# Kernel tuning notes

Measured on AMD Instinct MI355X. Metric: run time of the kernel, lower is better.

The kernel has to match this reference:

```python
import jax, jax.numpy as jnp
import numpy as np

B, H, W = 8, 64, 64
D_MODEL, D_STATE, D_INNER, DT_RANK, K = 96, 16, 192, 6, 4
EPS = 1e-6


def setup_inputs() -> dict:
    key = jax.random.key(0)
    ks = jax.random.split(key, 9)
    f = lambda k, s, sc=0.02: jax.random.normal(k, s, dtype=jnp.float32) * sc
    return {
        "x": jax.random.normal(ks[0], (B, H, W, D_MODEL), jnp.float32),
        "in_proj_w": f(ks[1], (2 * D_INNER, D_MODEL)),
        "conv_w": f(ks[2], (D_INNER, 1, 3, 3), 0.1),
        "conv_b": jnp.zeros((D_INNER,), jnp.float32),
        "x_proj_w": f(ks[3], (K * (DT_RANK + 2 * D_STATE), D_INNER)),
        "dt_projs_w": f(ks[4], (K * D_INNER, DT_RANK), 0.1),
        "A_logs": jnp.log(jax.random.uniform(ks[5], (K * D_INNER, D_STATE), jnp.float32, 1.0, 16.0)),
        "Ds": jnp.ones((K * D_INNER,), jnp.float32),
        "dt_projs_bias": f(ks[6], (K * D_INNER,), 0.5),
        "norm_w": jnp.ones((D_INNER,), jnp.float32),
        "norm_b": jnp.zeros((D_INNER,), jnp.float32),
        "out_proj_w": f(ks[7], (D_MODEL, D_INNER)),
    }


def _ss2d(x, in_proj_w, conv_w, conv_b, x_proj_w, dt_projs_w, A_logs, Ds,
          dt_projs_bias, norm_w, norm_b, out_proj_w):
    silu = jax.nn.silu
    Bb, Hh, Ww, _ = x.shape
    L = Hh * Ww
    # in_proj, split x/z, z gate activation
    xz = x @ in_proj_w.T                                   # (B,H,W,2*Di)
    xx, z = jnp.split(xz, 2, axis=-1)
    z = silu(z)
    # depthwise conv 3x3 in NCHW
    xc = jnp.transpose(xx, (0, 3, 1, 2))                   # (B,Di,H,W)
    xc = jax.lax.conv_general_dilated(
        xc, conv_w, (1, 1), ((1, 1), (1, 1)),
        dimension_numbers=("NCHW", "OIHW", "NCHW"),
        feature_group_count=D_INNER) + conv_b[None, :, None, None]
    xc = silu(xc)
    # 4-way cross scan: hw, wh (transposed), and their reversals
    x_hw = xc.reshape(Bb, D_INNER, L)
    x_wh = jnp.transpose(xc, (0, 1, 3, 2)).reshape(Bb, D_INNER, L)
    xs = jnp.stack([x_hw, x_wh, x_hw[..., ::-1], x_wh[..., ::-1]], axis=1)  # (B,K,Di,L)
    # per-group projections for dt, B, C
    xpw = x_proj_w.reshape(K, DT_RANK + 2 * D_STATE, D_INNER)
    x_dbl = jnp.einsum("bkdl,kcd->bkcl", xs, xpw)
    dts, Bs, Cs = jnp.split(x_dbl, [DT_RANK, DT_RANK + D_STATE], axis=2)
    dtw = dt_projs_w.reshape(K, D_INNER, DT_RANK)
    dts = jnp.einsum("bkrl,kdr->bkdl", dts, dtw)           # (B,K,Di,L)
    A = -jnp.exp(A_logs).reshape(K, D_INNER, D_STATE)      # (K,Di,N)
    dt = jax.nn.softplus(dts + dt_projs_bias.reshape(1, K, D_INNER, 1))
    # selective scan over L
    def step(h, inp):
        u_t, dt_t, B_t, C_t = inp                          # (B,K,Di),(B,K,Di),(B,K,N),(B,K,N)
        dA = jnp.exp(dt_t[..., None] * A)                  # (B,K,Di,N)
        h = h * dA + (dt_t * u_t)[..., None] * B_t[:, :, None, :]
        y = jnp.einsum("bkdn,bkn->bkd", h, C_t)
        return h, y
    h0 = jnp.zeros((Bb, K, D_INNER, D_STATE), jnp.float32)
    seq = (jnp.moveaxis(xs, -1, 0), jnp.moveaxis(dt, -1, 0),
           jnp.moveaxis(Bs, -1, 0), jnp.moveaxis(Cs, -1, 0))
    _, ysL = jax.lax.scan(step, h0, seq)
    ys = jnp.moveaxis(ysL, 0, -1)                          # (B,K,Di,L)
    ys = ys + xs * Ds.reshape(1, K, D_INNER, 1)
    # cross merge: invert flips and wh-transpose, then sum the 4 directions
    y = ys[:, 0] + ys[:, 2][..., ::-1]
    yw = ys[:, 1] + ys[:, 3][..., ::-1]
    y = y + yw.reshape(Bb, D_INNER, Ww, Hh).transpose(0, 1, 3, 2).reshape(Bb, D_INNER, L)
    y = y.reshape(Bb, D_INNER, Hh, Ww).transpose(0, 2, 3, 1)   # (B,H,W,Di)
    # out LayerNorm over channels
    mean = y.mean(-1, keepdims=True)
    var = ((y - mean) ** 2).mean(-1, keepdims=True)
    y = (y - mean) / jnp.sqrt(var + EPS) * norm_w + norm_b
    # gate and out_proj
    y = y * z
    return y @ out_proj_w.T                                # (B,H,W,d_model)


def reference(x, in_proj_w, conv_w, conv_b, x_proj_w, dt_projs_w, A_logs, Ds,
              dt_projs_bias, norm_w, norm_b, out_proj_w):
    return _ss2d(x, in_proj_w, conv_w, conv_b, x_proj_w, dt_projs_w, A_logs, Ds,
                 dt_projs_bias, norm_w, norm_b, out_proj_w)
```

## Files before the change

### kernel.cpp

```cpp
#include <hip/hip_runtime.h>
#include <hip/hip_bf16.h>
#include <math.h>

#define BB 8
#define HS 64
#define WS 64
#define LL 4096
#define DM 96
#define DI 192
#define NS 16
#define RR 6
#define KK 4
#define NCH 64
#define LC 64
#define XP 16
#define EPSN 1e-6f

typedef __attribute__((ext_vector_type(2))) float f32x2;

__device__ __forceinline__ float fsilu(float x) { return x / (1.f + __expf(-x)); }
__device__ __forceinline__ float rexp2(float x) {
    float r; asm("v_exp_f32 %0, %1" : "=v"(r) : "v"(x)); return r;
}
__device__ __forceinline__ float rlog2(float x) {
    float r; asm("v_log_f32 %0, %1" : "=v"(r) : "v"(x)); return r;
}
__device__ __forceinline__ f32x2 pk_mul(f32x2 a, f32x2 b) {
    f32x2 d; asm("v_pk_mul_f32 %0, %1, %2" : "=v"(d) : "v"(a), "v"(b)); return d;
}
__device__ __forceinline__ f32x2 pk_fma(f32x2 a, f32x2 b, f32x2 c) {
    f32x2 d; asm("v_pk_fma_f32 %0, %1, %2, %3" : "=v"(d) : "v"(a), "v"(b), "v"(c)); return d;
}
__device__ __forceinline__ float fsoftplus(float x) {
    float t = rexp2(x * 1.44269504f);
    float r = 0.69314718f * rlog2(1.f + t);
    return (x > 20.f) ? x : r;
}
__device__ __forceinline__ int lmap(int k, int t) {
    int tt = (k >= 2) ? (LL - 1 - t) : t;
    if (k & 1) tt = ((tt & 63) << 6) | (tt >> 6);
    return tt;
}

__global__ __launch_bounds__(192) void k_inproj(const float* __restrict__ x,
        const float* __restrict__ Win, float* __restrict__ xx, float* __restrict__ zs) {
    __shared__ __align__(16) float xrow[8][96];
    int p0 = blockIdx.x * 8;
    int tid = threadIdx.x;
    {
        const float4* src = (const float4*)(x + (size_t)p0 * 96);
        float4* dst = (float4*)&xrow[0][0];
        dst[tid] = src[tid];
    }
    __syncthreads();
    const float4* wr0 = (const float4*)(Win + (size_t)tid * 96);
    const float4* wr1 = (const float4*)(Win + (size_t)(tid + DI) * 96);
    f32x2 acc[8];
    #pragma unroll
    for (int p = 0; p < 8; ++p) acc[p] = (f32x2){0.f, 0.f};
    #pragma unroll 6
    for (int i = 0; i < 24; ++i) {
        float4 w0 = wr0[i];
        float4 w1 = wr1[i];
        f32x2 wx = {w0.x, w1.x}, wy = {w0.y, w1.y}, wz = {w0.z, w1.z}, ww = {w0.w, w1.w};
        #pragma unroll
        for (int p = 0; p < 8; ++p) {
            float4 x4 = *(const float4*)&xrow[p][i * 4];
            acc[p] = pk_fma(wx, (f32x2){x4.x, x4.x}, acc[p]);
            acc[p] = pk_fma(wy, (f32x2){x4.y, x4.y}, acc[p]);
            acc[p] = pk_fma(wz, (f32x2){x4.z, x4.z}, acc[p]);
            acc[p] = pk_fma(ww, (f32x2){x4.w, x4.w}, acc[p]);
        }
    }
    #pragma unroll
    for (int p = 0; p < 8; ++p) {
        xx[(size_t)(p0 + p) * DI + tid] = acc[p].x;
        zs[(size_t)(p0 + p) * DI + tid] = fsilu(acc[p].y);
    }
}

__global__ __launch_bounds__(256) void k_conv(const float* __restrict__ xx,
        const float* __restrict__ cw, const float* __restrict__ cb,
        float* __restrict__ xc) {
    int idx = blockIdx.x * 256 + threadIdx.x;
    int d = idx % DI; int P = idx / DI;
    int l = P & (LL - 1); int h = l >> 6; int w = l & 63;
    float acc = cb[d];
    #pragma unroll
    for (int i = 0; i < 3; ++i) {
        int hh = h + i - 1;
        if ((unsigned)hh < 64u) {
            #pragma unroll
            for (int j = 0; j < 3; ++j) {
                int ww = w + j - 1;
                if ((unsigned)ww < 64u)
                    acc += xx[(size_t)(P + (i - 1) * 64 + (j - 1)) * DI + d] * cw[d * 9 + i * 3 + j];
            }
        }
    }
    xc[idx] = fsilu(acc);
}

__global__ __launch_bounds__(192) void k_xdbl(const float* __restrict__ xc,
        const float* __restrict__ xpw, float* __restrict__ dts_raw,
        float* __restrict__ Bs, float* __restrict__ Cs) {
    __shared__ __align__(16) float xt[XP][DI];
    int tid = threadIdx.x;
    int p0 = blockIdx.x * XP;
    {
        const float4* src = (const float4*)(xc + (size_t)p0 * DI);
        float4* dst = (float4*)&xt[0][0];
        #pragma unroll
        for (int e = 0; e < XP * DI / 4 / 192; ++e) dst[tid + e * 192] = src[tid + e * 192];
    }
    __syncthreads();
    int c = tid;
    int k = c / 38, c2 = c % 38;
    const float4* w4p = (const float4*)(xpw + (size_t)c * DI);
    float acc[XP];
    #pragma unroll
    for (int p = 0; p < XP; ++p) acc[p] = 0.f;
    if (c < 152) {
        #pragma unroll 4
        for (int i = 0; i < DI / 4; ++i) {
            float4 w4 = w4p[i];
            #pragma unroll
            for (int p = 0; p < XP; ++p) {
                float4 x4 = *(const float4*)&xt[p][i * 4];
                acc[p] += w4.x * x4.x + w4.y * x4.y + w4.z * x4.z + w4.w * x4.w;
            }
        }
        #pragma unroll
        for (int p = 0; p < XP; ++p) {
            int P = p0 + p;
            int b = P >> 12; int l = P & (LL - 1);
            int lt = ((l & 63) << 6) | (l >> 6);
            int tk = (k == 0) ? l : (k == 1) ? lt : (k == 2) ? (LL - 1 - l) : (LL - 1 - lt);
            size_t it = ((size_t)(b * KK + k) * LL + tk);
            if (c2 < RR)            dts_raw[it * RR + c2] = acc[p];
            else if (c2 < RR + NS)  Bs[it * NS + (c2 - RR)] = acc[p];
            else                    Cs[it * NS + (c2 - RR - NS)] = acc[p];
        }
    }
}

__global__ __launch_bounds__(192) void k_scan1(const float* __restrict__ xc,
        const float* __restrict__ dts_raw, const float* __restrict__ Bsg,
        const float* __restrict__ A_logs, const float* __restrict__ dtw,
        const float* __restrict__ dtb,
        float* __restrict__ asum_g, float* __restrict__ hpart) {
    int bi = blockIdx.x;
    int b = bi >> 8; int rem = bi & 255; int k = rem >> 6; int c0 = rem & 63;
    int t0 = c0 * LC;
    int d = threadIdx.x;
    size_t g0 = (size_t)(b * KK + k) * LL + t0;
    const float2* dg = (const float2*)(dts_raw + g0 * RR);
    const float4* bg = (const float4*)(Bsg + g0 * NS);
    int kd = k * DI + d;
    f32x2 Ar2v[8];
    #pragma unroll
    for (int n2 = 0; n2 < 8; ++n2) {
        Ar2v[n2].x = -__expf(A_logs[(size_t)kd * NS + 2 * n2]) * 1.44269504f;
        Ar2v[n2].y = -__expf(A_logs[(size_t)kd * NS + 2 * n2 + 1]) * 1.44269504f;
    }
    f32x2 dw2[3];
    #pragma unroll
    for (int r = 0; r < 3; ++r) { dw2[r].x = dtw[kd * RR + 2 * r]; dw2[r].y = dtw[kd * RR + 2 * r + 1]; }
    float bias = dtb[kd];
    f32x2 h2[8];
    #pragma unroll
    for (int n2 = 0; n2 < 8; ++n2) h2[n2] = (f32x2){0.f, 0.f};
    float asum = 0.f;
    const float* xcb = xc + (size_t)b * LL * DI + d;
    float uu[4];
    #pragma unroll
    for (int j = 0; j < 4; ++j) uu[j] = xcb[(size_t)lmap(k, t0 + j) * DI];
    for (int tg = 0; tg < LC; tg += 4) {
        float un[4];
        int tb = t0 + ((tg + 4 < LC) ? (tg + 4) : tg);
        #pragma unroll
        for (int j = 0; j < 4; ++j) un[j] = xcb[(size_t)lmap(k, tb + j) * DI];
        #pragma unroll
        for (int j = 0; j < 4; ++j) {
            int t = tg + j;
            float2 q01 = dg[t * 3], q23 = dg[t * 3 + 1], q45 = dg[t * 3 + 2];
            f32x2 a2 = pk_mul((f32x2){q01.x, q01.y}, dw2[0]);
            a2 = pk_fma((f32x2){q23.x, q23.y}, dw2[1], a2);
            a2 = pk_fma((f32x2){q45.x, q45.y}, dw2[2], a2);
            float dt = fsoftplus(bias + a2.x + a2.y);
            asum += dt;
            float dtu = dt * uu[j];
            f32x2 dt2 = {dt, dt}, dtu2 = {dtu, dtu};
            #pragma unroll
            for (int n4 = 0; n4 < 4; ++n4) {
                float4 b4 = bg[t * 4 + n4];
                f32x2 tl = pk_mul(dt2, Ar2v[n4 * 2]);
                f32x2 th = pk_mul(dt2, Ar2v[n4 * 2 + 1]);
                f32x2 el = {rexp2(tl.x), rexp2(tl.y)};
                f32x2 eh = {rexp2(th.x), rexp2(th.y)};
                h2[n4 * 2]     = pk_fma(h2[n4 * 2],     el, pk_mul(dtu2, (f32x2){b4.x, b4.y}));
                h2[n4 * 2 + 1] = pk_fma(h2[n4 * 2 + 1], eh, pk_mul(dtu2, (f32x2){b4.z, b4.w}));
            }
        }
        #pragma unroll
        for (int j = 0; j < 4; ++j) uu[j] = un[j];
    }
    asum_g[(size_t)bi * DI + d] = asum;
    size_t base = ((size_t)bi * DI + d) * NS;
    #pragma unroll
    for (int n4 = 0; n4 < 4; ++n4) {
        float4 hv = make_float4(h2[n4 * 2].x, h2[n4 * 2].y, h2[n4 * 2 + 1].x, h2[n4 * 2 + 1].y);
        *(float4*)&hpart[base + n4 * 4] = hv;
    }
}

__global__ __launch_bounds__(256) void k_mid(const float* __restrict__ asum_g,
        const float* __restrict__ A_logs, float* __restrict__ hpp) {
    int g = blockIdx.x * 256 + threadIdx.x;
    int bk = g / (DI * NS);
    int rem = g % (DI * NS);
    int d = rem >> 4; int n = rem & 15;
    int k = bk & 3;
    float Ar2 = -__expf(A_logs[(size_t)(k * DI + d) * NS + n]) * 1.44269504f;
    float h = 0.f;
    for (int c = 0; c < NCH; ++c) {
        size_t row = (size_t)(bk * NCH + c) * DI + d;
        float a = rexp2(Ar2 * asum_g[row]);
        size_t ix = row * NS + n;
        float hp = hpp[ix];
        hpp[ix] = h;
        h = a * h + hp;
    }
}

__global__ __launch_bounds__(192) void k_scan2(const float* __restrict__ xc,
        const float* __restrict__ dts_raw, const float* __restrict__ Bsg,
        const float* __restrict__ Csg, const float* __restrict__ A_logs,
        const float* __restrict__ dtw, const float* __restrict__ dtb,
        const float* __restrict__ hinb, float* __restrict__ ysb) {
    int bi = blockIdx.x;
    int b = bi >> 8; int rem = bi & 255; int k = rem >> 6; int c0 = rem & 63;
    int t0 = c0 * LC;
    int d = threadIdx.x;
    size_t g0 = (size_t)(b * KK + k) * LL + t0;
    const float2* dg = (const float2*)(dts_raw + g0 * RR);
    const float4* bg = (const float4*)(Bsg + g0 * NS);
    const float4* cg = (const float4*)(Csg + g0 * NS);
    int kd = k * DI + d;
    f32x2 Ar2v[8];
    #pragma unroll
    for (int n2 = 0; n2 < 8; ++n2) {
        Ar2v[n2].x = -__expf(A_logs[(size_t)kd * NS + 2 * n2]) * 1.44269504f;
        Ar2v[n2].y = -__expf(A_logs[(size_t)kd * NS + 2 * n2 + 1]) * 1.44269504f;
    }
    f32x2 dw2[3];
    #pragma unroll
    for (int r = 0; r < 3; ++r) { dw2[r].x = dtw[kd * RR + 2 * r]; dw2[r].y = dtw[kd * RR + 2 * r + 1]; }
    float bias = dtb[kd];
    size_t base = ((size_t)bi * DI + d) * NS;
    f32x2 h2[8];
    #pragma unroll
    for (int n4 = 0; n4 < 4; ++n4) {
        float4 hv = *(const float4*)&hinb[base + n4 * 4];
        h2[n4 * 2]     = (f32x2){hv.x, hv.y};
        h2[n4 * 2 + 1] = (f32x2){hv.z, hv.w};
    }
    const float* xcb = xc + (size_t)b * LL * DI + d;
    float* ysw = ysb + g0 * DI + d;
    float uu[4];
    #pragma unroll
    for (int j = 0; j < 4; ++j) uu[j] = xcb[(size_t)lmap(k, t0 + j) * DI];
    for (int tg = 0; tg < LC; tg += 4) {
        float un[4];
        int tb = t0 + ((tg + 4 < LC) ? (tg + 4) : tg);
        #pragma unroll
        for (int j = 0; j < 4; ++j) un[j] = xcb[(size_t)lmap(k, tb + j) * DI];
        #pragma unroll
        for (int j = 0; j < 4; ++j) {
            int t = tg + j;
            float2 q01 = dg[t * 3], q23 = dg[t * 3 + 1], q45 = dg[t * 3 + 2];
            f32x2 a2 = pk_mul((f32x2){q01.x, q01.y}, dw2[0]);
            a2 = pk_fma((f32x2){q23.x, q23.y}, dw2[1], a2);
            a2 = pk_fma((f32x2){q45.x, q45.y}, dw2[2], a2);
            float dt = fsoftplus(bias + a2.x + a2.y);
            float dtu = dt * uu[j];
            f32x2 dt2 = {dt, dt}, dtu2 = {dtu, dtu};
            f32x2 y2 = {0.f, 0.f};
            #pragma unroll
            for (int n4 = 0; n4 < 4; ++n4) {
                float4 b4 = bg[t * 4 + n4];
                float4 c4 = cg[t * 4 + n4];
                f32x2 tl = pk_mul(dt2, Ar2v[n4 * 2]);
                f32x2 th = pk_mul(dt2, Ar2v[n4 * 2 + 1]);
                f32x2 el = {rexp2(tl.x), rexp2(tl.y)};
                f32x2 eh = {rexp2(th.x), rexp2(th.y)};
                h2[n4 * 2]     = pk_fma(h2[n4 * 2],     el, pk_mul(dtu2, (f32x2){b4.x, b4.y}));
                h2[n4 * 2 + 1] = pk_fma(h2[n4 * 2 + 1], eh, pk_mul(dtu2, (f32x2){b4.z, b4.w}));
                y2 = pk_fma(h2[n4 * 2],     (f32x2){c4.x, c4.y}, y2);
                y2 = pk_fma(h2[n4 * 2 + 1], (f32x2){c4.z, c4.w}, y2);
            }
            ysw[(size_t)t * DI] = y2.x + y2.y;
        }
        #pragma unroll
        for (int j = 0; j < 4; ++j) uu[j] = un[j];
    }
}

__global__ __launch_bounds__(256) void k_final(const float* __restrict__ xc,
        const float* __restrict__ ysb, const float* __restrict__ Ds,
        const float* __restrict__ zs, const float* __restrict__ nw,
        const float* __restrict__ nb, const float* __restrict__ Wout,
        float* __restrict__ out) {
    __shared__ __align__(16) float gs[32][DI];
    int tid = threadIdx.x;
    int wv = tid >> 6, lane = tid & 63;
    int Pbase = blockIdx.x * 32;
    float nwv[3], nbv[3], sdv[3];
    #pragma unroll
    for (int j = 0; j < 3; ++j) {
        int c = lane + 64 * j;
        nwv[j] = nw[c]; nbv[j] = nb[c];
        sdv[j] = Ds[c] + Ds[DI + c] + Ds[2 * DI + c] + Ds[3 * DI + c];
    }
    for (int pi = 0; pi < 8; ++pi) {
        int pl = wv * 8 + pi;
        int P = Pbase + pl;
        int b = P >> 12, l = P & (LL - 1);
        size_t Poff = (size_t)P * DI;
        size_t r0 = ((size_t)(b * KK + 0) * LL + lmap(0, l)) * DI;
        size_t r1 = ((size_t)(b * KK + 1) * LL + lmap(1, l)) * DI;
        size_t r2 = ((size_t)(b * KK + 2) * LL + lmap(2, l)) * DI;
        size_t r3 = ((size_t)(b * KK + 3) * LL + lmap(3, l)) * DI;
        float v[3];
        #pragma unroll
        for (int j = 0; j < 3; ++j) {
            int c = lane + 64 * j;
            v[j] = xc[Poff + c] * sdv[j]
                 + ysb[r0 + c] + ysb[r1 + c] + ysb[r2 + c] + ysb[r3 + c];
        }
        float s = v[0] + v[1] + v[2];
        #pragma unroll
        for (int o = 32; o; o >>= 1) s += __shfl_xor(s, o);
        float mean = s * (1.f / 192.f);
        float ss = 0.f;
        #pragma unroll
        for (int j = 0; j < 3; ++j) { float dd = v[j] - mean; ss += dd * dd; }
        #pragma unroll
        for (int o = 32; o; o >>= 1) ss += __shfl_xor(ss, o);
        float rstd = rsqrtf(ss * (1.f / 192.f) + EPSN);
        #pragma unroll
        for (int j = 0; j < 3; ++j) {
            int c = lane + 64 * j;
            gs[pl][c] = ((v[j] - mean) * rstd * nwv[j] + nbv[j]) * zs[Poff + c];
        }
    }
    __syncthreads();
    int o = tid & 127;
    int pg = tid >> 7;
    if (o < DM) {
        const float* wr = Wout + (size_t)o * DI;
        float acc[16];
        #pragma unroll
        for (int p = 0; p < 16; ++p) acc[p] = 0.f;
        for (int k0 = 0; k0 < DI; k0 += 4) {
            float4 w4 = *(const float4*)(wr + k0);
            #pragma unroll
            for (int p = 0; p < 16; ++p) {
                float4 g4 = *(const float4*)(&gs[pg * 16 + p][k0]);
                acc[p] += w4.x * g4.x + w4.y * g4.y + w4.z * g4.z + w4.w * g4.w;
            }
        }
        #pragma unroll
        for (int p = 0; p < 16; ++p)
            out[(size_t)(Pbase + pg * 16 + p) * DM + o] = acc[p];
    }
}

extern "C" void kernel_launch(void* const* d_in, const int* in_sizes, int n_in,
                              void* d_out, int out_size, void* d_ws, size_t ws_size,
                              hipStream_t stream) {
    const float* x      = (const float*)d_in[0];
    const float* in_w   = (const float*)d_in[1];
    const float* conv_w = (const float*)d_in[2];
    const float* conv_b = (const float*)d_in[3];
    const float* xpw    = (const float*)d_in[4];
    const float* dtw    = (const float*)d_in[5];
    const float* A_logs = (const float*)d_in[6];
    const float* Ds     = (const float*)d_in[7];
    const float* dtb    = (const float*)d_in[8];
    const float* nw     = (const float*)d_in[9];
    const float* nb     = (const float*)d_in[10];
    const float* out_w  = (const float*)d_in[11];
    float* out = (float*)d_out;

    char* ws = (char*)d_ws;
    size_t off = 0;
    auto alloc = [&](size_t n) { float* p = (float*)(ws + off); off += n * sizeof(float); return p; };
    float* zs   = alloc((size_t)BB * LL * DI);
    float* xc   = alloc((size_t)BB * LL * DI);
    float* dts  = alloc((size_t)BB * KK * LL * RR);
    float* Bsb  = alloc((size_t)BB * KK * LL * NS);
    float* Csb  = alloc((size_t)BB * KK * LL * NS);
    float* asum = alloc((size_t)BB * KK * NCH * DI);
    float* hpp  = alloc((size_t)BB * KK * NCH * DI * NS);
    float* ysb  = alloc((size_t)BB * KK * LL * DI);
    float* xx   = ysb;

    k_inproj<<<BB * LL / 8, 192, 0, stream>>>(x, in_w, xx, zs);
    k_conv<<<BB * LL * DI / 256, 256, 0, stream>>>(xx, conv_w, conv_b, xc);
    k_xdbl<<<BB * LL / XP, 192, 0, stream>>>(xc, xpw, dts, Bsb, Csb);
    k_scan1<<<BB * KK * NCH, DI, 0, stream>>>(xc, dts, Bsb, A_logs, dtw, dtb, asum, hpp);
    k_mid<<<(BB * KK * DI * NS) / 256, 256, 0, stream>>>(asum, A_logs, hpp);
    k_scan2<<<BB * KK * NCH, DI, 0, stream>>>(xc, dts, Bsb, Csb, A_logs, dtw, dtb, hpp, ysb);
    k_final<<<BB * LL / 32, 256, 0, stream>>>(xc, ysb, Ds, zs, nw, nb, out_w, out);
}
```

Before: 516.2 us.

## Retile in_proj kernel to 32 pixels per block with 4x16 register tile

The input projection kernel now processes 32 pixels per block instead of 8, and each thread computes 4 output channels for 16 pixels instead of 2 channels for 8 pixels. This cuts weight reloads from global or L2 per pixel and raises arithmetic per load. It drops the packed FMA asm in favour of scalar FMAs. It also uses 64 accumulator registers, which may lower occupancy, and the grid shrinks to 1024 blocks.

New measurement: 450.3 us. -12.8%, faster.

```diff
diff --git a/kernel.cpp b/kernel.cpp
--- a/kernel.cpp
+++ b/kernel.cpp
@@ -44,38 +44,43 @@
 
 __global__ __launch_bounds__(192) void k_inproj(const float* __restrict__ x,
         const float* __restrict__ Win, float* __restrict__ xx, float* __restrict__ zs) {
-    __shared__ __align__(16) float xrow[8][96];
-    int p0 = blockIdx.x * 8;
+    __shared__ __align__(16) float xrow[32][96];
+    int p0 = blockIdx.x * 32;
     int tid = threadIdx.x;
     {
         const float4* src = (const float4*)(x + (size_t)p0 * 96);
         float4* dst = (float4*)&xrow[0][0];
-        dst[tid] = src[tid];
+        #pragma unroll
+        for (int e = 0; e < 4; ++e) dst[tid + e * 192] = src[tid + e * 192];
     }
     __syncthreads();
-    const float4* wr0 = (const float4*)(Win + (size_t)tid * 96);
-    const float4* wr1 = (const float4*)(Win + (size_t)(tid + DI) * 96);
-    f32x2 acc[8];
-    #pragma unroll
-    for (int p = 0; p < 8; ++p) acc[p] = (f32x2){0.f, 0.f};
-    #pragma unroll 6
+    int c = tid % 96;
+    int pg = tid / 96;
+    const float4* w0 = (const float4*)(Win + (size_t)c * 96);
+    const float4* w1 = (const float4*)(Win + (size_t)(c + 96) * 96);
+    const float4* w2 = (const float4*)(Win + (size_t)(c + 192) * 96);
+    const float4* w3 = (const float4*)(Win + (size_t)(c + 288) * 96);
+    float a0v[16], a1v[16], a2v[16], a3v[16];
+    #pragma unroll
+    for (int p = 0; p < 16; ++p) { a0v[p] = 0.f; a1v[p] = 0.f; a2v[p] = 0.f; a3v[p] = 0.f; }
     for (int i = 0; i < 24; ++i) {
-        float4 w0 = wr0[i];
-        float4 w1 = wr1[i];
-        f32x2 wx = {w0.x, w1.x}, wy = {w0.y, w1.y}, wz = {w0.z, w1.z}, ww = {w0.w, w1.w};
-        #pragma unroll
-        for (int p = 0; p < 8; ++p) {
-            float4 x4 = *(const float4*)&xrow[p][i * 4];
-            acc[p] = pk_fma(wx, (f32x2){x4.x, x4.x}, acc[p]);
-            acc[p] = pk_fma(wy, (f32x2){x4.y, x4.y}, acc[p]);
-            acc[p] = pk_fma(wz, (f32x2){x4.z, x4.z}, acc[p]);
-            acc[p] = pk_fma(ww, (f32x2){x4.w, x4.w}, acc[p]);
-        }
-    }
-    #pragma unroll
-    for (int p = 0; p < 8; ++p) {
-        xx[(size_t)(p0 + p) * DI + tid] = acc[p].x;
-        zs[(size_t)(p0 + p) * DI + tid] = fsilu(acc[p].y);
+        float4 q0 = w0[i], q1 = w1[i], q2 = w2[i], q3 = w3[i];
+        #pragma unroll
+        for (int p = 0; p < 16; ++p) {
+            float4 x4 = *(const float4*)&xrow[pg * 16 + p][i * 4];
+            a0v[p] += q0.x * x4.x + q0.y * x4.y + q0.z * x4.z + q0.w * x4.w;
+            a1v[p] += q1.x * x4.x + q1.y * x4.y + q1.z * x4.z + q1.w * x4.w;
+            a2v[p] += q2.x * x4.x + q2.y * x4.y + q2.z * x4.z + q2.w * x4.w;
+            a3v[p] += q3.x * x4.x + q3.y * x4.y + q3.z * x4.z + q3.w * x4.w;
+        }
+    }
+    #pragma unroll
+    for (int p = 0; p < 16; ++p) {
+        size_t row = (size_t)(p0 + pg * 16 + p) * DI;
+        xx[row + c]      = a0v[p];
+        xx[row + c + 96] = a1v[p];
+        zs[row + c]      = fsilu(a2v[p]);
+        zs[row + c + 96] = fsilu(a3v[p]);
     }
 }
 
@@ -406,7 +411,7 @@
     float* ysb  = alloc((size_t)BB * KK * LL * DI);
     float* xx   = ysb;
 
-    k_inproj<<<BB * LL / 8, 192, 0, stream>>>(x, in_w, xx, zs);
+    k_inproj<<<BB * LL / 32, 192, 0, stream>>>(x, in_w, xx, zs);
     k_conv<<<BB * LL * DI / 256, 256, 0, stream>>>(xx, conv_w, conv_b, xc);
     k_xdbl<<<BB * LL / XP, 192, 0, stream>>>(xc, xpw, dts, Bsb, Csb);
     k_scan1<<<BB * KK * NCH, DI, 0, stream>>>(xc, dts, Bsb, A_logs, dtw, dtb, asum, hpp);
```
